# Kernel tuning notes

Measured on AMD Instinct MI355X. Metric: run time of the kernel, lower is better.

The kernel has to match this reference:

```python
import jax, jax.numpy as jnp
import numpy as np

N_NODES = 100000
K_HOPS = 2


def _gcn_norm(edge_index, edge_weight, num_nodes, fill_value=1.0):
    # renorm trick: add self-loops with weight fill_value, then D^-1/2 A D^-1/2
    row, col = edge_index[0], edge_index[1]
    sl = jnp.arange(num_nodes, dtype=edge_index.dtype)
    row = jnp.concatenate([row, sl])
    col = jnp.concatenate([col, sl])
    w = jnp.concatenate([edge_weight, jnp.full((num_nodes,), fill_value, edge_weight.dtype)])
    deg = jax.ops.segment_sum(w, row, num_segments=num_nodes)
    dinv = jnp.where(deg > 0, jax.lax.rsqrt(deg), 0.0)
    normed_w = dinv[row] * w * dinv[col]
    return row, col, normed_w


def setup_inputs() -> dict:
    key = jax.random.key(0)
    k1, k2, k3 = jax.random.split(key, 3)
    n_edges, d, units = 1000000, 64, 64
    x = jax.random.normal(k1, (N_NODES, d), dtype=jnp.float32)
    edge_index = jax.random.randint(k2, (2, n_edges), 0, N_NODES, dtype=jnp.int32)
    edge_weight = jnp.ones((n_edges,), dtype=jnp.float32)
    kernel = jax.random.normal(k3, (d, units), dtype=jnp.float32) * (1.0 / np.sqrt(d))
    bias = jnp.zeros((units,), dtype=jnp.float32)
    return {"x": x, "edge_index": edge_index, "edge_weight": edge_weight,
            "kernel": kernel, "bias": bias}


def reference(x, edge_index, edge_weight, kernel, bias):
    # SGC: K-hop normalized sparse propagation, then single dense linear
    row, col, w = _gcn_norm(edge_index, edge_weight, N_NODES, fill_value=1.0)
    h = x
    for _ in range(K_HOPS):
        h = jax.ops.segment_sum(w[:, None] * h[col], row, num_segments=N_NODES)
    out = h @ kernel + bias  # activation=None
    return out
```

## Files before the change

### kernel.cpp

```cpp
#include <hip/hip_runtime.h>


constexpr int kN = 100000;
constexpr int kD = 64;
constexpr int BSHIFT = 9;
constexpr int NBUCK = (kN + 511) >> BSHIFT;
constexpr int CHUNK = 4096;
constexpr int XW_ROWS = 128;
constexpr int ECW_PAD = 256;

__device__ __forceinline__ unsigned short f2bf(float f) {
    unsigned b = __float_as_uint(f);
    b += 0x7FFF + ((b >> 16) & 1);
    return (unsigned short)(b >> 16);
}
__device__ __forceinline__ float lo16(unsigned u) {
    return __uint_as_float(u << 16);
}
__device__ __forceinline__ float hi16(unsigned u) {
    return __uint_as_float(u & 0xffff0000u);
}

__global__ __launch_bounds__(256) void k_xw_count(const float* __restrict__ x,
                                                  const float* __restrict__ W,
                                                  unsigned short* __restrict__ y,
                                                  const int* __restrict__ row,
                                                  int* __restrict__ bc,
                                                  int* __restrict__ done,
                                                  int nxw, int nblk, int n, int E) {
    __shared__ float Xs[XW_ROWS][kD];
    int bid = blockIdx.x;
    int t = threadIdx.x;
    if (bid == 0 && t == 0) *done = 0;
    if (bid >= nxw) {
        int cb = bid - nxw;
        int* hist = (int*)&Xs[0][0];
        hist[t] = 0;
        __syncthreads();
        int g0 = cb * CHUNK;
        int nn = min(CHUNK, E - g0);
        for (int i = t; i < nn; i += 256) {
            atomicAdd(&hist[row[g0 + i] >> BSHIFT], 1);
        }
        __syncthreads();
        if (t < NBUCK) bc[t * nblk + cb] = hist[t];
        return;
    }
    int lane = t & 63;
    int wv = t >> 6;
    int row0 = bid * XW_ROWS;
    float Wc[kD];
#pragma unroll
    for (int k = 0; k < kD; ++k) Wc[k] = W[k * kD + lane];
    for (int i = t; i < XW_ROWS * (kD / 4); i += 256) {
        int r = i >> 4;
        int q = i & 15;
        float4 v = make_float4(0.0f, 0.0f, 0.0f, 0.0f);
        if (row0 + r < n)
            v = *reinterpret_cast<const float4*>(x + (size_t)(row0 + r) * kD + q * 4);
        *reinterpret_cast<float4*>(&Xs[r][q * 4]) = v;
    }
    __syncthreads();
    int rbase = wv * 32;
#pragma unroll
    for (int rr = 0; rr < 32; rr += 2) {
        int r0 = rbase + rr;
        float acc0 = 0.0f, acc1 = 0.0f;
#pragma unroll
        for (int q = 0; q < 16; ++q) {
            float4 a = *reinterpret_cast<const float4*>(&Xs[r0][q * 4]);
            float4 b = *reinterpret_cast<const float4*>(&Xs[r0 + 1][q * 4]);
            acc0 = fmaf(a.x, Wc[q * 4 + 0], acc0);
            acc1 = fmaf(b.x, Wc[q * 4 + 0], acc1);
            acc0 = fmaf(a.y, Wc[q * 4 + 1], acc0);
            acc1 = fmaf(b.y, Wc[q * 4 + 1], acc1);
            acc0 = fmaf(a.z, Wc[q * 4 + 2], acc0);
            acc1 = fmaf(b.z, Wc[q * 4 + 2], acc1);
            acc0 = fmaf(a.w, Wc[q * 4 + 3], acc0);
            acc1 = fmaf(b.w, Wc[q * 4 + 3], acc1);
        }
        int gr = row0 + r0;
        if (gr < n) y[(size_t)gr * kD + lane] = f2bf(acc0);
        if (gr + 1 < n) y[(size_t)(gr + 1) * kD + lane] = f2bf(acc1);
    }
}

__global__ __launch_bounds__(256) void kA_scan(int* __restrict__ bc,
                                               int* __restrict__ tot,
                                               int* __restrict__ base,
                                               int2* __restrict__ ecw_pad,
                                               int* __restrict__ done, int nblk) {
    __shared__ int sh[256];
    __shared__ int lastflag;
    int b = blockIdx.x;
    int t = threadIdx.x;
    int* p = bc + (size_t)b * nblk;
    int ipt = (nblk + 255) >> 8;
    int s0 = t * ipt;
    int s1 = min(s0 + ipt, nblk);
    int lsum = 0;
    for (int k = s0; k < s1; ++k) lsum += p[k];
    sh[t] = lsum;
    __syncthreads();
    for (int off = 1; off < 256; off <<= 1) {
        int add = (t >= off) ? sh[t - off] : 0;
        __syncthreads();
        sh[t] += add;
        __syncthreads();
    }
    int run = sh[t] - lsum;
    for (int k = s0; k < s1; ++k) {
        int v = p[k];
        p[k] = run;
        run += v;
    }
    if (t == 255) tot[b] = sh[255];
    __threadfence();
    __syncthreads();
    if (t == 0) lastflag = (atomicAdd(done, 1) == NBUCK - 1);
    __syncthreads();
    if (lastflag) {
        int v = (t < NBUCK) ? atomicAdd(&tot[t], 0) : 0;
        sh[t] = v;
        __syncthreads();
        for (int off = 1; off < 256; off <<= 1) {
            int add = (t >= off) ? sh[t - off] : 0;
            __syncthreads();
            sh[t] += add;
            __syncthreads();
        }
        if (t < NBUCK) base[t] = sh[t] - v;
        ecw_pad[t] = make_int2(0, 0);
    }
}

__global__ __launch_bounds__(256) void kA_place(const int* __restrict__ row,
                                                const int* __restrict__ col,
                                                const float* __restrict__ w,
                                                const int* __restrict__ bc,
                                                const int* __restrict__ base, int nblk,
                                                int2* __restrict__ tmp, int E) {
    __shared__ int hist[256];
    __shared__ int lbase[256];
    __shared__ int gb[256];
    __shared__ int cur[256];
    __shared__ int2 stage[CHUNK];
    __shared__ unsigned char bkt[CHUNK];
    int t = threadIdx.x;
    hist[t] = 0;
    __syncthreads();
    int g0 = blockIdx.x * CHUNK;
    int n = min(CHUNK, E - g0);
    for (int i = t; i < n; i += 256) {
        atomicAdd(&hist[row[g0 + i] >> BSHIFT], 1);
    }
    __syncthreads();
    int v = hist[t];
    lbase[t] = v;
    __syncthreads();
    for (int off = 1; off < 256; off <<= 1) {
        int add = (t >= off) ? lbase[t - off] : 0;
        __syncthreads();
        lbase[t] += add;
        __syncthreads();
    }
    int excl = lbase[t] - v;
    __syncthreads();
    lbase[t] = excl;
    cur[t] = excl;
    if (t < NBUCK) gb[t] = base[t] + bc[t * nblk + blockIdx.x];
    __syncthreads();
    for (int i = t; i < n; i += 256) {
        int r = row[g0 + i];
        int c = col[g0 + i];
        float wv = w[g0 + i];
        int b = r >> BSHIFT;
        int lp = atomicAdd(&cur[b], 1);
        stage[lp] = make_int2(c | ((r & 511) << 17), __float_as_int(wv));
        bkt[lp] = (unsigned char)b;
    }
    __syncthreads();
    for (int i = t; i < n; i += 256) {
        int b = bkt[i];
        tmp[gb[b] + (i - lbase[b])] = stage[i];
    }
}

__global__ __launch_bounds__(512) void kD_deg(const int2* __restrict__ tmp,
                                              const int* __restrict__ base,
                                              float* __restrict__ dinv, int E) {
    __shared__ float degs[512];
    int b = blockIdx.x;
    int t = threadIdx.x;
    degs[t] = 0.0f;
    __syncthreads();
    int gbase = base[b];
    int gend = (b == NBUCK - 1) ? E : base[b + 1];
    int node0 = b << BSHIFT;
    int nloc = min(512, kN - node0);
    for (int i = gbase + t; i < gend; i += 512) {
        int2 e = tmp[i];
        atomicAdd(&degs[(e.x >> 17) & 511], __int_as_float(e.y));
    }
    __syncthreads();
    if (t < nloc) {
        float d = 1.0f + degs[t];
        dinv[node0 + t] = (d > 0.0f) ? rsqrtf(d) : 0.0f;
    }
}

__global__ __launch_bounds__(512) void kB_sort(const int2* __restrict__ tmp,
                                               const int* __restrict__ base,
                                               const float* __restrict__ dinv,
                                               int2* __restrict__ ecw,
                                               int* __restrict__ start, int E) {
    __shared__ int hist[512];
    __shared__ int cur[512];
    int b = blockIdx.x;
    int t = threadIdx.x;
    int gbase = base[b];
    int gend = (b == NBUCK - 1) ? E : base[b + 1];
    int size = gend - gbase;
    int node0 = b << BSHIFT;
    int nloc = min(512, kN - node0);
    hist[t] = 0;
    __syncthreads();
    for (int i = t; i < size; i += 512) {
        atomicAdd(&hist[(tmp[gbase + i].x >> 17) & 511], 1);
    }
    __syncthreads();
    int v = hist[t];
    hist[t] = v;
    __syncthreads();
    for (int off = 1; off < 512; off <<= 1) {
        int add = (t >= off) ? hist[t - off] : 0;
        __syncthreads();
        hist[t] += add;
        __syncthreads();
    }
    int excl = hist[t] - v;
    __syncthreads();
    cur[t] = excl;
    __syncthreads();
    if (t < nloc) start[node0 + t] = gbase + excl;
    if (b == 0 && t == 0) start[kN] = E;
    for (int i = t; i < size; i += 512) {
        int2 e = tmp[gbase + i];
        int c = e.x & 0x1FFFF;
        int rl = (e.x >> 17) & 511;
        float wn = dinv[node0 + rl] * __int_as_float(e.y) * dinv[c];
        int lp = atomicAdd(&cur[rl], 1);
        ecw[gbase + lp] = make_int2(c << 7, __float_as_int(wn));
    }
}

template <typename OutWriter>
__device__ __forceinline__ void hop_body(const int* __restrict__ start,
                                         const int2* __restrict__ ecw,
                                         const float* __restrict__ dinv,
                                         const unsigned short* __restrict__ h_in,
                                         int n, OutWriter writeout) {
    int wv = threadIdx.x >> 6;
    int lane = threadIdx.x & 63;
    int g = lane >> 3;
    int f = lane & 7;
    int node = blockIdx.x * 32 + wv * 8 + g;
    bool valid = node < n;
    int nd = valid ? node : (n - 1);
    const char* hb = (const char*)h_in;
    int lo = f << 4;
    float di = dinv[nd];
    float d2 = di * di;
    uint4 su = *(const uint4*)(hb + ((size_t)nd << 7) + lo);
    float a0 = d2 * lo16(su.x), a1 = d2 * hi16(su.x);
    float a2 = d2 * lo16(su.y), a3 = d2 * hi16(su.y);
    float a4 = d2 * lo16(su.z), a5 = d2 * hi16(su.z);
    float a6 = d2 * lo16(su.w), a7 = d2 * hi16(su.w);
    int s = start[nd], e = start[nd + 1];
    int d = e - s;
    int m = max(d, __shfl_xor(d, 8));
    m = max(m, __shfl_xor(m, 16));
    int dmax = max(m, __shfl_xor(m, 32));
    for (int it = 0; it < dmax; it += 4) {
        int j = s + it;
        int2 v0 = ecw[j + 0];
        int2 v1 = ecw[j + 1];
        int2 v2 = ecw[j + 2];
        int2 v3 = ecw[j + 3];
        bool p0 = (it + 0 < d), p1 = (it + 1 < d);
        bool p2 = (it + 2 < d), p3 = (it + 3 < d);
        unsigned o0 = p0 ? (unsigned)v0.x : 0u;
        unsigned o1 = p1 ? (unsigned)v1.x : 0u;
        unsigned o2 = p2 ? (unsigned)v2.x : 0u;
        unsigned o3 = p3 ? (unsigned)v3.x : 0u;
        uint4 g0 = *(const uint4*)(hb + (o0 + lo));
        uint4 g1 = *(const uint4*)(hb + (o1 + lo));
        uint4 g2 = *(const uint4*)(hb + (o2 + lo));
        uint4 g3 = *(const uint4*)(hb + (o3 + lo));
        float w0 = p0 ? __int_as_float(v0.y) : 0.0f;
        float w1 = p1 ? __int_as_float(v1.y) : 0.0f;
        float w2 = p2 ? __int_as_float(v2.y) : 0.0f;
        float w3 = p3 ? __int_as_float(v3.y) : 0.0f;
        a0 = fmaf(w0, lo16(g0.x), a0); a1 = fmaf(w0, hi16(g0.x), a1);
        a2 = fmaf(w0, lo16(g0.y), a2); a3 = fmaf(w0, hi16(g0.y), a3);
        a4 = fmaf(w0, lo16(g0.z), a4); a5 = fmaf(w0, hi16(g0.z), a5);
        a6 = fmaf(w0, lo16(g0.w), a6); a7 = fmaf(w0, hi16(g0.w), a7);
        a0 = fmaf(w1, lo16(g1.x), a0); a1 = fmaf(w1, hi16(g1.x), a1);
        a2 = fmaf(w1, lo16(g1.y), a2); a3 = fmaf(w1, hi16(g1.y), a3);
        a4 = fmaf(w1, lo16(g1.z), a4); a5 = fmaf(w1, hi16(g1.z), a5);
        a6 = fmaf(w1, lo16(g1.w), a6); a7 = fmaf(w1, hi16(g1.w), a7);
        a0 = fmaf(w2, lo16(g2.x), a0); a1 = fmaf(w2, hi16(g2.x), a1);
        a2 = fmaf(w2, lo16(g2.y), a2); a3 = fmaf(w2, hi16(g2.y), a3);
        a4 = fmaf(w2, lo16(g2.z), a4); a5 = fmaf(w2, hi16(g2.z), a5);
        a6 = fmaf(w2, lo16(g2.w), a6); a7 = fmaf(w2, hi16(g2.w), a7);
        a0 = fmaf(w3, lo16(g3.x), a0); a1 = fmaf(w3, hi16(g3.x), a1);
        a2 = fmaf(w3, lo16(g3.y), a2); a3 = fmaf(w3, hi16(g3.y), a3);
        a4 = fmaf(w3, lo16(g3.z), a4); a5 = fmaf(w3, hi16(g3.z), a5);
        a6 = fmaf(w3, lo16(g3.w), a6); a7 = fmaf(w3, hi16(g3.w), a7);
    }
    if (valid) writeout(node, f, a0, a1, a2, a3, a4, a5, a6, a7);
}

__global__ __launch_bounds__(256) void k_hop1(const int* __restrict__ start,
                                              const int2* __restrict__ ecw,
                                              const float* __restrict__ dinv,
                                              const unsigned short* __restrict__ h_in,
                                              uint4* __restrict__ h_out, int n) {
    hop_body(start, ecw, dinv, h_in, n,
             [=](int node, int f, float a0, float a1, float a2, float a3,
                 float a4, float a5, float a6, float a7) {
                 uint4 p;
                 p.x = (unsigned)f2bf(a0) | ((unsigned)f2bf(a1) << 16);
                 p.y = (unsigned)f2bf(a2) | ((unsigned)f2bf(a3) << 16);
                 p.z = (unsigned)f2bf(a4) | ((unsigned)f2bf(a5) << 16);
                 p.w = (unsigned)f2bf(a6) | ((unsigned)f2bf(a7) << 16);
                 h_out[((size_t)node << 3) + f] = p;
             });
}

__global__ __launch_bounds__(256) void k_hop2(const int* __restrict__ start,
                                              const int2* __restrict__ ecw,
                                              const float* __restrict__ dinv,
                                              const unsigned short* __restrict__ h_in,
                                              const float* __restrict__ bias,
                                              float* __restrict__ out, int n) {
    hop_body(start, ecw, dinv, h_in, n,
             [=](int node, int f, float a0, float a1, float a2, float a3,
                 float a4, float a5, float a6, float a7) {
                 const float4* bp = reinterpret_cast<const float4*>(bias + (f << 3));
                 float4 b0 = bp[0], b1 = bp[1];
                 float4* op = reinterpret_cast<float4*>(out + ((size_t)node << 6) + (f << 3));
                 op[0] = make_float4(a0 + b0.x, a1 + b0.y, a2 + b0.z, a3 + b0.w);
                 op[1] = make_float4(a4 + b1.x, a5 + b1.y, a6 + b1.z, a7 + b1.w);
             });
}

extern "C" void kernel_launch(void* const* d_in, const int* in_sizes, int n_in,
                              void* d_out, int out_size, void* d_ws, size_t ws_size,
                              hipStream_t stream) {
    const float* x    = (const float*)d_in[0];
    const int*   ei   = (const int*)d_in[1];
    const float* ew   = (const float*)d_in[2];
    const float* W    = (const float*)d_in[3];
    const float* bias = (const float*)d_in[4];
    const int E = in_sizes[1] / 2;
    const int* row = ei;
    const int* col = ei + E;

    const int nblk = (E + CHUNK - 1) / CHUNK;
    const int nxw  = (kN + XW_ROWS - 1) / XW_ROWS;

    char* ws = (char*)d_ws;
    auto alloc = [&](size_t bytes) {
        char* p = ws;
        ws += ((bytes + 1023) & ~(size_t)1023);
        return p;
    };
    int*            base  = (int*)alloc(sizeof(int) * 256);
    int*            tot   = (int*)alloc(sizeof(int) * 256);
    int*            done  = (int*)alloc(sizeof(int) * 64);
    int*            bc    = (int*)alloc(sizeof(int) * (size_t)NBUCK * nblk);
    int*            start = (int*)alloc(sizeof(int) * (kN + 1));
    float*          dinv  = (float*)alloc(sizeof(float) * kN);
    int2*           ecw   = (int2*)alloc(sizeof(int2) * (size_t)(E + ECW_PAD));
    unsigned short* y     = (unsigned short*)alloc(sizeof(short) * (size_t)kN * kD);
    unsigned short* h1    = (unsigned short*)alloc(sizeof(short) * (size_t)kN * kD);
    int2*           tmp   = (int2*)h1;

    k_xw_count<<<nxw + nblk, 256, 0, stream>>>(x, W, y, row, bc, done,
                                               nxw, nblk, kN, E);

    kA_scan<<<NBUCK, 256, 0, stream>>>(bc, tot, base, ecw + E, done, nblk);
    kA_place<<<nblk, 256, 0, stream>>>(row, col, ew, bc, base, nblk, tmp, E);
    kD_deg<<<NBUCK, 512, 0, stream>>>(tmp, base, dinv, E);
    kB_sort<<<NBUCK, 512, 0, stream>>>(tmp, base, dinv, ecw, start, E);

    k_hop1<<<(kN + 31) / 32, 256, 0, stream>>>(start, ecw, dinv, y,
                                               (uint4*)h1, kN);
    k_hop2<<<(kN + 31) / 32, 256, 0, stream>>>(start, ecw, dinv, h1, bias,
                                               (float*)d_out, kN);
}
```

Baseline: 130.3 us.

## Degree-sort nodes within buckets and use 16 lanes per node in hops

kB_sort now counting-sorts the nodes of each 512-node bucket by in-degree and writes a permutation. The hop kernels visit nodes in that order, so the four nodes sharing a wavefront have similar degrees and less of the loop runs up to a wavefront-wide max that most nodes do not need. Each node now uses 16 lanes with 8-byte gathers instead of 8 lanes with 16-byte gathers. This halves nodes per wave and doubles the grid, and adds an extra scan pass in the sort plus an indirect perm load in each hop.

```diff
diff --git a/kernel.cpp b/kernel.cpp
--- a/kernel.cpp
+++ b/kernel.cpp
@@ -213,9 +213,11 @@
                                                const int* __restrict__ base,
                                                const float* __restrict__ dinv,
                                                int2* __restrict__ ecw,
-                                               int* __restrict__ start, int E) {
+                                               int* __restrict__ start,
+                                               int* __restrict__ perm, int E) {
     __shared__ int hist[512];
     __shared__ int cur[512];
+    __shared__ int deg[512];
     int b = blockIdx.x;
     int t = threadIdx.x;
     int gbase = base[b];
@@ -230,6 +232,7 @@
     }
     __syncthreads();
     int v = hist[t];
+    deg[t] = v;
     hist[t] = v;
     __syncthreads();
     for (int off = 1; off < 512; off <<= 1) {
@@ -252,6 +255,28 @@
         int lp = atomicAdd(&cur[rl], 1);
         ecw[gbase + lp] = make_int2(c << 7, __float_as_int(wn));
     }
+    __syncthreads();
+    hist[t] = 0;
+    __syncthreads();
+    int db = min(deg[t], 511);
+    if (t < nloc) atomicAdd(&hist[db], 1);
+    __syncthreads();
+    int v2 = hist[t];
+    __syncthreads();
+    for (int off = 1; off < 512; off <<= 1) {
+        int add = (t >= off) ? hist[t - off] : 0;
+        __syncthreads();
+        hist[t] += add;
+        __syncthreads();
+    }
+    int dexcl = hist[t] - v2;
+    __syncthreads();
+    cur[t] = dexcl;
+    __syncthreads();
+    if (t < nloc) {
+        int pos = atomicAdd(&cur[db], 1);
+        perm[node0 + pos] = node0 + t;
+    }
 }
 
 template <typename OutWriter>
@@ -259,28 +284,28 @@
                                          const int2* __restrict__ ecw,
                                          const float* __restrict__ dinv,
                                          const unsigned short* __restrict__ h_in,
+                                         const int* __restrict__ perm,
                                          int n, OutWriter writeout) {
     int wv = threadIdx.x >> 6;
     int lane = threadIdx.x & 63;
-    int g = lane >> 3;
-    int f = lane & 7;
-    int node = blockIdx.x * 32 + wv * 8 + g;
-    bool valid = node < n;
-    int nd = valid ? node : (n - 1);
+    int q = lane >> 4;
+    int f = lane & 15;
+    int slot = blockIdx.x * 16 + wv * 4 + q;
+    bool valid = slot < n;
+    int nd = perm[min(slot, n - 1)];
     const char* hb = (const char*)h_in;
-    int lo = f << 4;
+    int lo = f << 3;
     float di = dinv[nd];
     float d2 = di * di;
-    uint4 su = *(const uint4*)(hb + ((size_t)nd << 7) + lo);
-    float a0 = d2 * lo16(su.x), a1 = d2 * hi16(su.x);
-    float a2 = d2 * lo16(su.y), a3 = d2 * hi16(su.y);
-    float a4 = d2 * lo16(su.z), a5 = d2 * hi16(su.z);
-    float a6 = d2 * lo16(su.w), a7 = d2 * hi16(su.w);
+    uint2 su = *(const uint2*)(hb + ((size_t)nd << 7) + lo);
+    float acc0 = d2 * lo16(su.x);
+    float acc1 = d2 * hi16(su.x);
+    float acc2 = d2 * lo16(su.y);
+    float acc3 = d2 * hi16(su.y);
     int s = start[nd], e = start[nd + 1];
     int d = e - s;
-    int m = max(d, __shfl_xor(d, 8));
-    m = max(m, __shfl_xor(m, 16));
-    int dmax = max(m, __shfl_xor(m, 32));
+    int m1 = max(d, __shfl_xor(d, 16));
+    int dmax = max(m1, __shfl_xor(m1, 32));
     for (int it = 0; it < dmax; it += 4) {
         int j = s + it;
         int2 v0 = ecw[j + 0];
@@ -293,48 +318,46 @@
         unsigned o1 = p1 ? (unsigned)v1.x : 0u;
         unsigned o2 = p2 ? (unsigned)v2.x : 0u;
         unsigned o3 = p3 ? (unsigned)v3.x : 0u;
-        uint4 g0 = *(const uint4*)(hb + (o0 + lo));
-        uint4 g1 = *(const uint4*)(hb + (o1 + lo));
-        uint4 g2 = *(const uint4*)(hb + (o2 + lo));
-        uint4 g3 = *(const uint4*)(hb + (o3 + lo));
+        uint2 g0 = *(const uint2*)(hb + (o0 + lo));
+        uint2 g1 = *(const uint2*)(hb + (o1 + lo));
+        uint2 g2 = *(const uint2*)(hb + (o2 + lo));
+        uint2 g3 = *(const uint2*)(hb + (o3 + lo));
         float w0 = p0 ? __int_as_float(v0.y) : 0.0f;
         float w1 = p1 ? __int_as_float(v1.y) : 0.0f;
         float w2 = p2 ? __int_as_float(v2.y) : 0.0f;
         float w3 = p3 ? __int_as_float(v3.y) : 0.0f;
-        a0 = fmaf(w0, lo16(g0.x), a0); a1 = fmaf(w0, hi16(g0.x), a1);
-        a2 = fmaf(w0, lo16(g0.y), a2); a3 = fmaf(w0, hi16(g0.y), a3);
-        a4 = fmaf(w0, lo16(g0.z), a4); a5 = fmaf(w0, hi16(g0.z), a5);
-        a6 = fmaf(w0, lo16(g0.w), a6); a7 = fmaf(w0, hi16(g0.w), a7);
-        a0 = fmaf(w1, lo16(g1.x), a0); a1 = fmaf(w1, hi16(g1.x), a1);
-        a2 = fmaf(w1, lo16(g1.y), a2); a3 = fmaf(w1, hi16(g1.y), a3);
-        a4 = fmaf(w1, lo16(g1.z), a4); a5 = fmaf(w1, hi16(g1.z), a5);
-        a6 = fmaf(w1, lo16(g1.w), a6); a7 = fmaf(w1, hi16(g1.w), a7);
-        a0 = fmaf(w2, lo16(g2.x), a0); a1 = fmaf(w2, hi16(g2.x), a1);
-        a2 = fmaf(w2, lo16(g2.y), a2); a3 = fmaf(w2, hi16(g2.y), a3);
-        a4 = fmaf(w2, lo16(g2.z), a4); a5 = fmaf(w2, hi16(g2.z), a5);
-        a6 = fmaf(w2, lo16(g2.w), a6); a7 = fmaf(w2, hi16(g2.w), a7);
-        a0 = fmaf(w3, lo16(g3.x), a0); a1 = fmaf(w3, hi16(g3.x), a1);
-        a2 = fmaf(w3, lo16(g3.y), a2); a3 = fmaf(w3, hi16(g3.y), a3);
-        a4 = fmaf(w3, lo16(g3.z), a4); a5 = fmaf(w3, hi16(g3.z), a5);
-        a6 = fmaf(w3, lo16(g3.w), a6); a7 = fmaf(w3, hi16(g3.w), a7);
-    }
-    if (valid) writeout(node, f, a0, a1, a2, a3, a4, a5, a6, a7);
+        acc0 = fmaf(w0, lo16(g0.x), acc0);
+        acc1 = fmaf(w0, hi16(g0.x), acc1);
+        acc2 = fmaf(w0, lo16(g0.y), acc2);
+        acc3 = fmaf(w0, hi16(g0.y), acc3);
+        acc0 = fmaf(w1, lo16(g1.x), acc0);
+        acc1 = fmaf(w1, hi16(g1.x), acc1);
+        acc2 = fmaf(w1, lo16(g1.y), acc2);
+        acc3 = fmaf(w1, hi16(g1.y), acc3);
+        acc0 = fmaf(w2, lo16(g2.x), acc0);
+        acc1 = fmaf(w2, hi16(g2.x), acc1);
+        acc2 = fmaf(w2, lo16(g2.y), acc2);
+        acc3 = fmaf(w2, hi16(g2.y), acc3);
+        acc0 = fmaf(w3, lo16(g3.x), acc0);
+        acc1 = fmaf(w3, hi16(g3.x), acc1);
+        acc2 = fmaf(w3, lo16(g3.y), acc2);
+        acc3 = fmaf(w3, hi16(g3.y), acc3);
+    }
+    if (valid) writeout(nd, f, acc0, acc1, acc2, acc3);
 }
 
 __global__ __launch_bounds__(256) void k_hop1(const int* __restrict__ start,
                                               const int2* __restrict__ ecw,
                                               const float* __restrict__ dinv,
                                               const unsigned short* __restrict__ h_in,
-                                              uint4* __restrict__ h_out, int n) {
-    hop_body(start, ecw, dinv, h_in, n,
-             [=](int node, int f, float a0, float a1, float a2, float a3,
-                 float a4, float a5, float a6, float a7) {
-                 uint4 p;
+                                              const int* __restrict__ perm,
+                                              uint2* __restrict__ h_out64, int n) {
+    hop_body(start, ecw, dinv, h_in, perm, n,
+             [=](int node, int f, float a0, float a1, float a2, float a3) {
+                 uint2 p;
                  p.x = (unsigned)f2bf(a0) | ((unsigned)f2bf(a1) << 16);
                  p.y = (unsigned)f2bf(a2) | ((unsigned)f2bf(a3) << 16);
-                 p.z = (unsigned)f2bf(a4) | ((unsigned)f2bf(a5) << 16);
-                 p.w = (unsigned)f2bf(a6) | ((unsigned)f2bf(a7) << 16);
-                 h_out[((size_t)node << 3) + f] = p;
+                 h_out64[((size_t)node << 4) + f] = p;
              });
 }
 
@@ -342,16 +365,14 @@
                                               const int2* __restrict__ ecw,
                                               const float* __restrict__ dinv,
                                               const unsigned short* __restrict__ h_in,
+                                              const int* __restrict__ perm,
                                               const float* __restrict__ bias,
                                               float* __restrict__ out, int n) {
-    hop_body(start, ecw, dinv, h_in, n,
-             [=](int node, int f, float a0, float a1, float a2, float a3,
-                 float a4, float a5, float a6, float a7) {
-                 const float4* bp = reinterpret_cast<const float4*>(bias + (f << 3));
-                 float4 b0 = bp[0], b1 = bp[1];
-                 float4* op = reinterpret_cast<float4*>(out + ((size_t)node << 6) + (f << 3));
-                 op[0] = make_float4(a0 + b0.x, a1 + b0.y, a2 + b0.z, a3 + b0.w);
-                 op[1] = make_float4(a4 + b1.x, a5 + b1.y, a6 + b1.z, a7 + b1.w);
+    hop_body(start, ecw, dinv, h_in, perm, n,
+             [=](int node, int f, float a0, float a1, float a2, float a3) {
+                 float4 b = *reinterpret_cast<const float4*>(bias + (f << 2));
+                 float4 o = make_float4(a0 + b.x, a1 + b.y, a2 + b.z, a3 + b.w);
+                 *reinterpret_cast<float4*>(out + ((size_t)node << 6) + (f << 2)) = o;
              });
 }
 
@@ -381,6 +402,7 @@
     int*            done  = (int*)alloc(sizeof(int) * 64);
     int*            bc    = (int*)alloc(sizeof(int) * (size_t)NBUCK * nblk);
     int*            start = (int*)alloc(sizeof(int) * (kN + 1));
+    int*            perm  = (int*)alloc(sizeof(int) * kN);
     float*          dinv  = (float*)alloc(sizeof(float) * kN);
     int2*           ecw   = (int2*)alloc(sizeof(int2) * (size_t)(E + ECW_PAD));
     unsigned short* y     = (unsigned short*)alloc(sizeof(short) * (size_t)kN * kD);
@@ -393,10 +415,10 @@
     kA_scan<<<NBUCK, 256, 0, stream>>>(bc, tot, base, ecw + E, done, nblk);
     kA_place<<<nblk, 256, 0, stream>>>(row, col, ew, bc, base, nblk, tmp, E);
     kD_deg<<<NBUCK, 512, 0, stream>>>(tmp, base, dinv, E);
-    kB_sort<<<NBUCK, 512, 0, stream>>>(tmp, base, dinv, ecw, start, E);
-
-    k_hop1<<<(kN + 31) / 32, 256, 0, stream>>>(start, ecw, dinv, y,
-                                               (uint4*)h1, kN);
-    k_hop2<<<(kN + 31) / 32, 256, 0, stream>>>(start, ecw, dinv, h1, bias,
-                                               (float*)d_out, kN);
-}
+    kB_sort<<<NBUCK, 512, 0, stream>>>(tmp, base, dinv, ecw, start, perm, E);
+
+    k_hop1<<<(kN + 15) / 16, 256, 0, stream>>>(start, ecw, dinv, y, perm,
+                                               (uint2*)h1, kN);
+    k_hop2<<<(kN + 15) / 16, 256, 0, stream>>>(start, ecw, dinv, h1, perm,
+                                               bias, (float*)d_out, kN);
+}
```

Result: slower. 148.6 us (+14.1%).
